# Kernel optimization log

Measured on AMD Instinct MI355X. Metric: run time of the kernel, lower is better.

Reference implementation:

```python
import jax, jax.numpy as jnp
import numpy as np

N_EXPERTS = 8
TOP_K = 2


def setup_inputs() -> dict:
    key = jax.random.key(0)
    k1, k2, k3, k4 = jax.random.split(key, 4)
    B, T, C, H, E = 2, 2048, 1024, 4096, N_EXPERTS
    x = jax.random.normal(k1, (B, T, C), dtype=jnp.float32)
    # weights scaled like standard init to keep activations well-behaved
    router_w = jax.random.normal(k2, (E, C), dtype=jnp.float32) * 0.02
    w1 = jax.random.normal(k3, (E, C, H), dtype=jnp.float32) * (1.0 / np.sqrt(C))
    w2 = jax.random.normal(k4, (E, H, C), dtype=jnp.float32) * (1.0 / np.sqrt(H))
    return {"x": x, "router_w": router_w, "w1": w1, "w2": w2}


def reference(x, router_w, w1, w2):
    B, T, C = x.shape
    E = N_EXPERTS
    xf = x.reshape(-1, C)                                   # [N, C], N = B*T
    logits = jnp.einsum('nc,ec->ne', xf, router_w)          # router (no bias)
    probs = jax.nn.softmax(logits, axis=-1)
    top_w, top_i = jax.lax.top_k(probs, TOP_K)              # [N, K]
    top_w = top_w / jnp.sum(top_w, axis=-1, keepdims=True)  # renormalize
    # combine weight per (token, expert): sum of top-k weights routed to e
    comb = jnp.einsum('nk,nke->ne', top_w, jax.nn.one_hot(top_i, E, dtype=xf.dtype))
    # dense all-expert compute (bias=False, exact GELU, dropout=0 at eval)
    h = jax.nn.gelu(jnp.einsum('nc,ech->enh', xf, w1), approximate=False)  # [E, N, H]
    y = jnp.einsum('enh,ehc->enc', h, w2)                   # [E, N, C]
    out = jnp.einsum('ne,enc->nc', comb, y)                 # weighted combine
    return out.reshape(B, T, C)
```

## Files before the change

### kernel.cpp

```cpp
#include <hip/hip_runtime.h>
#include <hip/hip_bf16.h>
#include <stdint.h>

#define NTOK 4096
#define CD   1024
#define HD   4096
#define NE   8
#define ECAP 1536

typedef __attribute__((ext_vector_type(8))) short bf16x8;
typedef __attribute__((ext_vector_type(4))) float f32x4;
typedef __attribute__((ext_vector_type(4))) unsigned short us4;

#define BARR() asm volatile("s_barrier" ::: "memory")
#define VM2() asm volatile("s_waitcnt vmcnt(2)" ::: "memory")
#define VM0() asm volatile("s_waitcnt vmcnt(0)" ::: "memory")

__device__ __forceinline__ unsigned short f2bf(float f){
  __hip_bfloat16 h = __float2bfloat16(f);
  return *reinterpret_cast<unsigned short*>(&h);
}

__global__ __launch_bounds__(256) void fused_pre(
    const float* __restrict__ x, const float* __restrict__ rw,
    const float* __restrict__ w1, const float* __restrict__ w2,
    unsigned short* __restrict__ x_bf, int* __restrict__ counts,
    int* __restrict__ g_tok, float* __restrict__ g_w,
    unsigned short* __restrict__ w1t, unsigned short* __restrict__ w2t){
  __shared__ float tile[64][65];
  int bid = blockIdx.x;
  int tid = threadIdx.x;

  if (bid < NTOK/4){
    int l = tid & 63, w = tid >> 6;
    int n = bid*4 + w;

    float4 xv[4];
    #pragma unroll
    for (int j = 0; j < 4; ++j)
      xv[j] = ((const float4*)(x + (size_t)n*CD))[l + j*64];

    #pragma unroll
    for (int j = 0; j < 4; ++j){
      us4 o; o.x = f2bf(xv[j].x); o.y = f2bf(xv[j].y); o.z = f2bf(xv[j].z); o.w = f2bf(xv[j].w);
      *(us4*)(x_bf + (size_t)n*CD + l*4 + j*256) = o;
    }

    const float4* rwv = (const float4*)rw;
    double le[NE];
    #pragma unroll
    for (int e = 0; e < NE; ++e){
      double p = 0.0;
      #pragma unroll
      for (int j = 0; j < 4; ++j){
        float4 rv = rwv[e*(CD/4) + l + j*64];
        p += (double)xv[j].x*rv.x + (double)xv[j].y*rv.y + (double)xv[j].z*rv.z + (double)xv[j].w*rv.w;
      }
      #pragma unroll
      for (int d = 32; d >= 1; d >>= 1) p += __shfl_xor(p, d);
      le[e] = p;
    }
    if (l == 0){
      double m = le[0];
      #pragma unroll
      for (int e = 1; e < NE; ++e) m = le[e] > m ? le[e] : m;
      double pe[NE];
      #pragma unroll
      for (int e = 0; e < NE; ++e) pe[e] = exp(le[e]-m);
      int i0 = 0;
      #pragma unroll
      for (int e = 1; e < NE; ++e) if (pe[e] > pe[i0]) i0 = e;
      int i1 = (i0 == 0) ? 1 : 0;
      #pragma unroll
      for (int e = 0; e < NE; ++e){ if (e == i0) continue; if (pe[e] > pe[i1]) i1 = e; }
      double w0 = pe[i0], w1v = pe[i1], wsum = w0 + w1v;
      int p0 = atomicAdd(&counts[i0], 1);
      g_tok[i0*ECAP + p0] = n;  g_w[i0*ECAP + p0] = (float)(w0/wsum);
      int p1 = atomicAdd(&counts[i1], 1);
      g_tok[i1*ECAP + p1] = n;  g_w[i1*ECAP + p1] = (float)(w1v/wsum);
    }
    return;
  }

  const float* ip; unsigned short* op; int R, S, s0, r0;
  if (bid < NTOK/4 + 8192){
    int t = bid - NTOK/4;
    int xx = t & 63, yy = (t >> 6) & 15, e = t >> 10;
    R = CD; S = HD;
    ip = w1 + (size_t)e*CD*HD; op = w1t + (size_t)e*CD*HD;
    s0 = xx*64; r0 = yy*64;
  } else {
    int t = bid - NTOK/4 - 8192;
    int xx = t & 15, yy = (t >> 4) & 63, e = t >> 10;
    R = HD; S = CD;
    ip = w2 + (size_t)e*CD*HD; op = w2t + (size_t)e*CD*HD;
    s0 = xx*64; r0 = yy*64;
  }
  #pragma unroll
  for (int i = 0; i < 4; ++i){
    int lin = i*256 + tid;
    int rr = lin >> 4, c4 = lin & 15;
    float4 v = *(const float4*)(ip + (size_t)(r0+rr)*S + s0 + c4*4);
    tile[rr][c4*4+0] = v.x; tile[rr][c4*4+1] = v.y;
    tile[rr][c4*4+2] = v.z; tile[rr][c4*4+3] = v.w;
  }
  __syncthreads();
  #pragma unroll
  for (int i = 0; i < 4; ++i){
    int lin = i*256 + tid;
    int ss = lin >> 4, rq = lin & 15;
    us4 o;
    o.x = f2bf(tile[rq*4+0][ss]);
    o.y = f2bf(tile[rq*4+1][ss]);
    o.z = f2bf(tile[rq*4+2][ss]);
    o.w = f2bf(tile[rq*4+3][ss]);
    *(us4*)(op + (size_t)(s0+ss)*R + r0 + rq*4) = o;
  }
}

template<int KLEN, int SPLITK, int EPI>
__global__ __launch_bounds__(512, 6) void gemm_ring3(
    const unsigned short* __restrict__ A_src,
    const unsigned short* __restrict__ B_src,
    unsigned short* __restrict__ h_out,
    float* __restrict__ outp,
    const int* __restrict__ g_tok,
    const float* __restrict__ g_w,
    const int* __restrict__ counts,
    int NDIM, int KSTRIDE){
  constexpr int NT = KLEN/32;
  constexpr int ZPX = (NE*SPLITK)/8;
  __shared__ alignas(128) char lds[49152];

  int GN = gridDim.x, GY = gridDim.y;
  int p  = blockIdx.x + GN*(blockIdx.y + GY*blockIdx.z);
  int k8 = p & 7;
  int i  = p >> 3;
  int s  = i / (GN*GY);
  int r  = i - s*(GN*GY);
  int y  = r % GY;
  int xb = r / GY;
  int z  = k8*ZPX + s;

  int e  = (SPLITK == 1) ? z : (z / SPLITK);
  int kz = (SPLITK == 1) ? 0 : (z % SPLITK);
  int n_e = counts[e];
  int m0 = y*128;
  if (m0 >= n_e) return;
  int n0 = xb*128;
  int g_base = e*ECAP;
  int kstart = kz*KLEN;

  int tid = threadIdx.x, l = tid & 63, w = tid >> 6;
  int wr = w >> 2, wc = w & 3;
  int lrow = l & 15, q = l >> 4;

  const unsigned short* src[2];
  uint32_t dst[2];
  #pragma unroll
  for (int ii = 0; ii < 2; ++ii){
    int g = ii*512 + tid;
    bool isA = g < 512;
    int gg = isA ? g : (g - 512);
    int row = gg >> 2, c = gg & 3;
    int cs = c ^ (row & 3) ^ ((row >> 2) & 3);
    if (isA){
      int rg = m0 + row; if (rg > n_e-1) rg = n_e-1;
      size_t arow;
      if (EPI == 0) arow = (size_t)g_tok[g_base + rg];
      else          arow = (size_t)(g_base + rg);
      src[ii] = A_src + arow*(size_t)KSTRIDE + kstart + cs*8;
    } else {
      src[ii] = B_src + ((size_t)e*NDIM + n0 + row)*(size_t)KSTRIDE + kstart + cs*8;
    }
    dst[ii] = (uint32_t)g*16u;
  }

  auto STAGE = [&](int tt, uint32_t bufoff){
    #pragma unroll
    for (int ii = 0; ii < 2; ++ii)
      __builtin_amdgcn_global_load_lds(
        (const __attribute__((address_space(1))) void*)(src[ii] + (size_t)tt*32),
        (__attribute__((address_space(3))) void*)&lds[dst[ii] + bufoff], 16, 0, 0);
  };

  uint32_t a_off[4], b_off[2];
  #pragma unroll
  for (int m = 0; m < 4; ++m){
    int ra = wr*64 + m*16 + lrow;
    int Xa = (ra & 3) ^ ((ra >> 2) & 3);
    a_off[m] = (uint32_t)(ra*64) + 16u*(uint32_t)(q ^ Xa);
  }
  #pragma unroll
  for (int n = 0; n < 2; ++n){
    int rb = wc*32 + n*16 + lrow;
    int Xb = (rb & 3) ^ ((rb >> 2) & 3);
    b_off[n] = 8192u + (uint32_t)(rb*64) + 16u*(uint32_t)(q ^ Xb);
  }

  f32x4 acc[4][2] = {};

  STAGE(0, 0u); STAGE(1, 16384u);

  uint32_t ro = 0u;
  uint32_t so = 32768u;
  #pragma unroll 1
  for (int kt = 0; kt < NT; ++kt){
    if (kt < NT-1) { VM2(); } else { VM0(); }
    BARR();
    if (kt + 2 < NT) STAGE(kt + 2, so);
    bf16x8 av[4], bv[2];
    #pragma unroll
    for (int m = 0; m < 4; ++m)
      av[m] = *(const bf16x8*)&lds[a_off[m] + ro];
    #pragma unroll
    for (int n = 0; n < 2; ++n)
      bv[n] = *(const bf16x8*)&lds[b_off[n] + ro];
    __builtin_amdgcn_s_setprio(1);
    #pragma unroll
    for (int m = 0; m < 4; ++m)
      #pragma unroll
      for (int n = 0; n < 2; ++n)
        acc[m][n] = __builtin_amdgcn_mfma_f32_16x16x32_bf16(av[m], bv[n], acc[m][n], 0, 0, 0);
    __builtin_amdgcn_s_setprio(0);
    ro = (ro == 32768u) ? 0u : ro + 16384u;
    so = (so == 32768u) ? 0u : so + 16384u;
  }

  if (EPI == 0){
    #pragma unroll
    for (int m = 0; m < 4; ++m){
      #pragma unroll
      for (int jj = 0; jj < 4; ++jj){
        int rr = m0 + wr*64 + m*16 + q*4 + jj;
        if (rr < n_e){
          unsigned short* hp = h_out + (size_t)(g_base + rr)*NDIM + n0 + wc*32 + lrow;
          #pragma unroll
          for (int n = 0; n < 2; ++n){
            float v = acc[m][n][jj];
            v = 0.5f*v*(1.0f + erff(v*0.70710678118654752f));
            hp[n*16] = f2bf(v);
          }
        }
      }
    }
  } else {
    #pragma unroll
    for (int m = 0; m < 4; ++m){
      #pragma unroll
      for (int jj = 0; jj < 4; ++jj){
        int rr = m0 + wr*64 + m*16 + q*4 + jj;
        if (rr < n_e){
          int slot = g_base + rr;
          int tt = g_tok[slot];
          float wgt = g_w[slot];
          float* op = outp + (size_t)tt*NDIM + n0 + wc*32 + lrow;
          #pragma unroll
          for (int n = 0; n < 2; ++n)
            atomicAdd(op + n*16, wgt*acc[m][n][jj]);
        }
      }
    }
  }
}

extern "C" void kernel_launch(void* const* d_in, const int* in_sizes, int n_in,
                              void* d_out, int out_size, void* d_ws, size_t ws_size,
                              hipStream_t stream) {
  const float* x  = (const float*)d_in[0];
  const float* rw = (const float*)d_in[1];
  const float* w1 = (const float*)d_in[2];
  const float* w2 = (const float*)d_in[3];

  size_t off = 0;
  auto alloc = [&](size_t sz) -> char* {
    char* p = (char*)d_ws + off;
    off += (sz + 255) & ~(size_t)255;
    return p;
  };
  unsigned short* x_bf = (unsigned short*)alloc((size_t)NTOK*CD*2);
  unsigned short* w1t  = (unsigned short*)alloc((size_t)NE*CD*HD*2);
  unsigned short* w2t  = (unsigned short*)alloc((size_t)NE*CD*HD*2);
  unsigned short* hbuf = (unsigned short*)alloc((size_t)NE*ECAP*HD*2);
  int*   counts = (int*)alloc(64);
  int*   g_tok  = (int*)alloc(NE*ECAP*4);
  float* g_w    = (float*)alloc(NE*ECAP*4);
  (void)ws_size; (void)in_sizes; (void)n_in; (void)out_size;

  hipMemsetAsync(d_out, 0, (size_t)NTOK*CD*4, stream);
  hipMemsetAsync(counts, 0, 64, stream);

  fused_pre<<<dim3(NTOK/4 + 8192 + 8192), dim3(256), 0, stream>>>(
      x, rw, w1, w2, x_bf, counts, g_tok, g_w, w1t, w2t);

  gemm_ring3<CD, 1, 0><<<dim3(HD/128, 12, NE), dim3(512), 0, stream>>>(
      x_bf, w1t, hbuf, (float*)nullptr, g_tok, g_w, counts, HD, CD);
  gemm_ring3<HD/2, 2, 1><<<dim3(CD/128, 12, NE*2), dim3(512), 0, stream>>>(
      hbuf, w2t, (unsigned short*)nullptr, (float*)d_out, g_tok, g_w, counts, CD, HD);
}
```

Measured before the change: 413.1 us.

## Overlap w2 transpose-convert with first expert GEMM by interleaving blocks

Moves the w2 fp32-to-bf16 transpose out of the preprocessing kernel and into the first GEMM launch. Extra blocks are interleaved with the GEMM blocks (16 of every 40) and each converts four 64x64 tiles with double-buffered LDS and 8-wide stores. The goal is to overlap the memory-bound w2 conversion with the compute-bound first GEMM. In exchange, the transpose blocks compete with GEMM blocks for occupancy and bandwidth, and the GEMM loses its early exit for empty row tiles only in ordering.

```diff
diff --git a/kernel.cpp b/kernel.cpp
--- a/kernel.cpp
+++ b/kernel.cpp
@@ -11,6 +11,7 @@
 typedef __attribute__((ext_vector_type(8))) short bf16x8;
 typedef __attribute__((ext_vector_type(4))) float f32x4;
 typedef __attribute__((ext_vector_type(4))) unsigned short us4;
+typedef __attribute__((ext_vector_type(8))) unsigned short us8;
 
 #define BARR() asm volatile("s_barrier" ::: "memory")
 #define VM2() asm volatile("s_waitcnt vmcnt(2)" ::: "memory")
@@ -23,10 +24,10 @@
 
 __global__ __launch_bounds__(256) void fused_pre(
     const float* __restrict__ x, const float* __restrict__ rw,
-    const float* __restrict__ w1, const float* __restrict__ w2,
+    const float* __restrict__ w1,
     unsigned short* __restrict__ x_bf, int* __restrict__ counts,
     int* __restrict__ g_tok, float* __restrict__ g_w,
-    unsigned short* __restrict__ w1t, unsigned short* __restrict__ w2t){
+    unsigned short* __restrict__ w1t){
   __shared__ float tile[64][65];
   int bid = blockIdx.x;
   int tid = threadIdx.x;
@@ -82,25 +83,16 @@
     return;
   }
 
-  const float* ip; unsigned short* op; int R, S, s0, r0;
-  if (bid < NTOK/4 + 8192){
-    int t = bid - NTOK/4;
-    int xx = t & 63, yy = (t >> 6) & 15, e = t >> 10;
-    R = CD; S = HD;
-    ip = w1 + (size_t)e*CD*HD; op = w1t + (size_t)e*CD*HD;
-    s0 = xx*64; r0 = yy*64;
-  } else {
-    int t = bid - NTOK/4 - 8192;
-    int xx = t & 15, yy = (t >> 4) & 63, e = t >> 10;
-    R = HD; S = CD;
-    ip = w2 + (size_t)e*CD*HD; op = w2t + (size_t)e*CD*HD;
-    s0 = xx*64; r0 = yy*64;
-  }
+  int t = bid - NTOK/4;
+  int xx = t & 63, yy = (t >> 6) & 15, e = t >> 10;
+  const float* ip = w1 + (size_t)e*CD*HD;
+  unsigned short* op = w1t + (size_t)e*CD*HD;
+  int s0 = xx*64, r0 = yy*64;
   #pragma unroll
   for (int i = 0; i < 4; ++i){
     int lin = i*256 + tid;
     int rr = lin >> 4, c4 = lin & 15;
-    float4 v = *(const float4*)(ip + (size_t)(r0+rr)*S + s0 + c4*4);
+    float4 v = *(const float4*)(ip + (size_t)(r0+rr)*HD + s0 + c4*4);
     tile[rr][c4*4+0] = v.x; tile[rr][c4*4+1] = v.y;
     tile[rr][c4*4+2] = v.z; tile[rr][c4*4+3] = v.w;
   }
@@ -114,11 +106,11 @@
     o.y = f2bf(tile[rq*4+1][ss]);
     o.z = f2bf(tile[rq*4+2][ss]);
     o.w = f2bf(tile[rq*4+3][ss]);
-    *(us4*)(op + (size_t)(s0+ss)*R + r0 + rq*4) = o;
+    *(us4*)(op + (size_t)(s0+ss)*CD + r0 + rq*4) = o;
   }
 }
 
-template<int KLEN, int SPLITK, int EPI>
+template<int KLEN, int SPLITK, int EPI, int FUSE>
 __global__ __launch_bounds__(512, 6) void gemm_ring3(
     const unsigned short* __restrict__ A_src,
     const unsigned short* __restrict__ B_src,
@@ -127,13 +119,61 @@
     const int* __restrict__ g_tok,
     const float* __restrict__ g_w,
     const int* __restrict__ counts,
-    int NDIM, int KSTRIDE){
+    int NDIM, int KSTRIDE, int GN, int GY,
+    const float* __restrict__ w2src, unsigned short* __restrict__ w2dst){
   constexpr int NT = KLEN/32;
   constexpr int ZPX = (NE*SPLITK)/8;
   __shared__ alignas(128) char lds[49152];
 
-  int GN = gridDim.x, GY = gridDim.y;
-  int p  = blockIdx.x + GN*(blockIdx.y + GY*blockIdx.z);
+  int bid = blockIdx.x + gridDim.x*(blockIdx.y + gridDim.y*blockIdx.z);
+  int tid = threadIdx.x;
+  int p;
+  if (FUSE){
+    int gp = bid/40, rm = bid%40;
+    if (rm >= 24){
+      typedef float ftile_t[64][65];
+      ftile_t* tiles = (ftile_t*)lds;
+      int base = (gp*16 + (rm - 24)) * 4;
+      float4 v[2];
+      auto LOADREGS = [&](int t){
+        int xx = t & 15, yy = (t >> 4) & 63, e = t >> 10;
+        const float* ip = w2src + (size_t)e*CD*HD;
+        #pragma unroll
+        for (int i = 0; i < 2; ++i){
+          int lin = i*512 + tid;
+          v[i] = *(const float4*)(ip + (size_t)(yy*64 + (lin>>4))*CD + xx*64 + (lin&15)*4);
+        }
+      };
+      LOADREGS(base);
+      #pragma unroll 1
+      for (int it = 0; it < 4; ++it){
+        float (*tile)[65] = tiles[it & 1];
+        #pragma unroll
+        for (int i = 0; i < 2; ++i){
+          int lin = i*512 + tid;
+          int rr2 = lin >> 4, c4 = lin & 15;
+          tile[rr2][c4*4+0] = v[i].x; tile[rr2][c4*4+1] = v[i].y;
+          tile[rr2][c4*4+2] = v[i].z; tile[rr2][c4*4+3] = v[i].w;
+        }
+        if (it < 3) LOADREGS(base + it + 1);
+        __syncthreads();
+        int t = base + it;
+        int xx = t & 15, yy = (t >> 4) & 63, e = t >> 10;
+        unsigned short* op = w2dst + (size_t)e*CD*HD;
+        int ss = tid >> 3, rq8 = tid & 7;
+        us8 o;
+        #pragma unroll
+        for (int j = 0; j < 8; ++j)
+          o[j] = f2bf(tile[rq8*8+j][ss]);
+        *(us8*)(op + (size_t)(xx*64+ss)*HD + yy*64 + rq8*8) = o;
+      }
+      return;
+    }
+    p = gp*24 + rm;
+  } else {
+    p = bid;
+  }
+
   int k8 = p & 7;
   int i  = p >> 3;
   int s  = i / (GN*GY);
@@ -151,7 +191,7 @@
   int g_base = e*ECAP;
   int kstart = kz*KLEN;
 
-  int tid = threadIdx.x, l = tid & 63, w = tid >> 6;
+  int l = tid & 63, w = tid >> 6;
   int wr = w >> 2, wc = w & 3;
   int lrow = l & 15, q = l >> 4;
 
@@ -290,11 +330,12 @@
   hipMemsetAsync(d_out, 0, (size_t)NTOK*CD*4, stream);
   hipMemsetAsync(counts, 0, 64, stream);
 
-  fused_pre<<<dim3(NTOK/4 + 8192 + 8192), dim3(256), 0, stream>>>(
-      x, rw, w1, w2, x_bf, counts, g_tok, g_w, w1t, w2t);
-
-  gemm_ring3<CD, 1, 0><<<dim3(HD/128, 12, NE), dim3(512), 0, stream>>>(
-      x_bf, w1t, hbuf, (float*)nullptr, g_tok, g_w, counts, HD, CD);
-  gemm_ring3<HD/2, 2, 1><<<dim3(CD/128, 12, NE*2), dim3(512), 0, stream>>>(
-      hbuf, w2t, (unsigned short*)nullptr, (float*)d_out, g_tok, g_w, counts, CD, HD);
+  fused_pre<<<dim3(NTOK/4 + 8192), dim3(256), 0, stream>>>(
+      x, rw, w1, x_bf, counts, g_tok, g_w, w1t);
+
+  gemm_ring3<CD, 1, 0, 1><<<dim3(5120), dim3(512), 0, stream>>>(
+      x_bf, w1t, hbuf, (float*)nullptr, g_tok, g_w, counts, HD, CD, 32, 12, w2, w2t);
+  gemm_ring3<HD/2, 2, 1, 0><<<dim3(8, 12, 16), dim3(512), 0, stream>>>(
+      hbuf, w2t, (unsigned short*)nullptr, (float*)d_out, g_tok, g_w, counts, CD, HD, 8, 12,
+      (const float*)nullptr, (unsigned short*)nullptr);
 }
```

Result: no change. 414.7 us (+0.4%).
